# Optimization experiments

Hardware: AMD Instinct MI355X
Metric: run time of the kernel (lower is better)

Reference implementation:

```python
import jax, jax.numpy as jnp
import numpy as np

B, S, D, H, HD, I, L = 1, 2048, 1024, 16, 64, 2816, 2
EPS = 1e-5
ROPE_BASE = 10000.0


def rmsnorm(x, w):
    return x * jax.lax.rsqrt(jnp.mean(x * x, axis=-1, keepdims=True) + EPS) * w


def precompute_freqs_cis():
    # matches precompute_freqs_cis: [S, HD//2, 2] = (cos, sin)
    freqs = 1.0 / (ROPE_BASE ** (jnp.arange(0, HD, 2, dtype=jnp.float32) / HD))
    ang = jnp.outer(jnp.arange(S, dtype=jnp.float32), freqs)
    return jnp.stack([jnp.cos(ang), jnp.sin(ang)], axis=-1)


def apply_rope(x, fc):
    # x: [B,S,H,HD]; fc: [S,HD//2,2] -> interleaved pair rotation
    xs = x.reshape(*x.shape[:-1], HD // 2, 2)
    f = fc[None, :, None]  # [1,S,1,HD//2,2]
    out = jnp.stack([
        xs[..., 0] * f[..., 0] - xs[..., 1] * f[..., 1],
        xs[..., 1] * f[..., 0] + xs[..., 0] * f[..., 1],
    ], axis=-1)
    return out.reshape(x.shape)


def setup_inputs() -> dict:
    key = jax.random.key(0)
    ks = jax.random.split(key, 6)
    p = lambda k, shape: jax.random.normal(k, shape, jnp.float32) * 0.02
    return {
        "x": jax.random.normal(ks[0], (B, S, D), jnp.float32),
        "wqkv": p(ks[1], (L, 3 * H * HD, D)),
        "wo": p(ks[2], (L, D, H * HD)),
        "w1": p(ks[3], (L, I, D)),
        "w2": p(ks[4], (L, D, I)),
        "w3": p(ks[5], (L, I, D)),
        "attn_norm_w": jnp.ones((L, D), jnp.float32),
        "ffn_norm_w": jnp.ones((L, D), jnp.float32),
        "attn_ls": 0.01 * jnp.ones((L, D), jnp.float32),
        "ffn_ls": 0.01 * jnp.ones((L, D), jnp.float32),
        "final_norm_w": jnp.ones((D,), jnp.float32),
    }


def reference(x, wqkv, wo, w1, w2, w3, attn_norm_w, ffn_norm_w, attn_ls, ffn_ls, final_norm_w):
    fc = precompute_freqs_cis()
    causal = jnp.tril(jnp.ones((S, S), dtype=bool))  # [S,S]
    scale = 1.0 / np.sqrt(HD).astype(np.float32)
    h = x
    for l in range(L):
        # --- attention block ---
        xn = rmsnorm(h, attn_norm_w[l])
        qkv = xn @ wqkv[l].T  # [B,S,3*H*HD]
        q, k, v = jnp.split(qkv, 3, axis=-1)
        q = apply_rope(q.reshape(B, S, H, HD), fc)
        k = apply_rope(k.reshape(B, S, H, HD), fc)
        v = v.reshape(B, S, H, HD)
        scores = jnp.einsum('bqhd,bkhd->bhqk', q, k) * scale
        scores = jnp.where(causal, scores, jnp.finfo(scores.dtype).min)
        attn = jax.nn.softmax(scores, axis=-1)
        y = jnp.einsum('bhqk,bkhd->bqhd', attn, v).reshape(B, S, H * HD)
        h = h + (y @ wo[l].T) * attn_ls[l]
        # --- feed-forward block (SwiGLU) ---
        xn = rmsnorm(h, ffn_norm_w[l])
        ff = (jax.nn.silu(xn @ w1[l].T) * (xn @ w3[l].T)) @ w2[l].T
        h = h + ff * ffn_ls[l]
    return rmsnorm(h, final_norm_w)
```

## Files before the change

kernel.cpp:

```cpp
#include <hip/hip_runtime.h>
#include <math.h>

#define SEQ 2048
#define DIM 1024
#define NH 16
#define HDIM 64
#define IDIM 2816
#define NL 2

typedef __attribute__((ext_vector_type(8))) short bf16x8;
typedef __attribute__((ext_vector_type(4))) float f32x4;

__device__ __forceinline__ unsigned short f2bf(float f) {
    unsigned int u = __float_as_uint(f);
    u = (u + 0x7fffu + ((u >> 16) & 1u)) >> 16;
    return (unsigned short)u;
}
__device__ __forceinline__ float bf2f(unsigned short u) {
    return __uint_as_float((unsigned int)u << 16);
}

__device__ __forceinline__ void gl_lds16(const void* g, void* l) {
    __builtin_amdgcn_global_load_lds(
        (const __attribute__((address_space(1))) unsigned int*)g,
        (__attribute__((address_space(3))) unsigned int*)l, 16, 0, 0);
}

#define WAITVM(n) asm volatile("s_waitcnt vmcnt(" #n ")" ::: "memory")
#define BARRIER_PIN()                       \
    do {                                    \
        __builtin_amdgcn_s_barrier();       \
        __builtin_amdgcn_sched_barrier(0);  \
    } while (0)

template <bool BF16OUT>
__global__ __launch_bounds__(256) void rmsnorm_kernel(const float* __restrict__ in,
                                                      const float* __restrict__ w,
                                                      void* __restrict__ out) {
    const int row = blockIdx.x;
    const int t = threadIdx.x;
    const float4 v = ((const float4*)(in + (size_t)row * DIM))[t];
    float ss = v.x * v.x + v.y * v.y + v.z * v.z + v.w * v.w;
#pragma unroll
    for (int m = 1; m < 64; m <<= 1) ss += __shfl_xor(ss, m);
    __shared__ float red[4];
    if ((t & 63) == 0) red[t >> 6] = ss;
    __syncthreads();
    const float tot = red[0] + red[1] + red[2] + red[3];
    const float r = 1.0f / sqrtf(tot * (1.0f / DIM) + 1e-5f);
    const float4 wv = ((const float4*)w)[t];
    float o0 = v.x * r * wv.x, o1 = v.y * r * wv.y;
    float o2 = v.z * r * wv.z, o3 = v.w * r * wv.w;
    if (BF16OUT) {
        ushort4 o = {f2bf(o0), f2bf(o1), f2bf(o2), f2bf(o3)};
        ((ushort4*)((unsigned short*)out + (size_t)row * DIM))[t] = o;
    } else {
        float4 o = {o0, o1, o2, o3};
        ((float4*)((float*)out + (size_t)row * DIM))[t] = o;
    }
}

#define WQKV_OFF 0
#define WO_OFF   3145728
#define W1_OFF   4194304
#define W3_OFF   7077888
#define W2_OFF   9961472
#define WTOT     12845056

__global__ __launch_bounds__(256) void convert_weights_kernel(
    const float* __restrict__ wqkv, const float* __restrict__ wo,
    const float* __restrict__ w1, const float* __restrict__ w3,
    const float* __restrict__ w2, unsigned short* __restrict__ out) {
    const size_t i8 = ((size_t)blockIdx.x * 256 + threadIdx.x) * 8;
    const float* src;
    size_t local;
    if (i8 < WO_OFF)      { src = wqkv; local = i8 - WQKV_OFF; }
    else if (i8 < W1_OFF) { src = wo;   local = i8 - WO_OFF; }
    else if (i8 < W3_OFF) { src = w1;   local = i8 - W1_OFF; }
    else if (i8 < W2_OFF) { src = w3;   local = i8 - W3_OFF; }
    else                  { src = w2;   local = i8 - W2_OFF; }
    const float4 v0 = *(const float4*)(src + local);
    const float4 v1 = *(const float4*)(src + local + 4);
    ushort4 o0 = {f2bf(v0.x), f2bf(v0.y), f2bf(v0.z), f2bf(v0.w)};
    ushort4 o1 = {f2bf(v1.x), f2bf(v1.y), f2bf(v1.z), f2bf(v1.w)};
    *(ushort4*)(out + i8) = o0;
    *(ushort4*)(out + i8 + 4) = o1;
}

template <int EPI, int BM, int BN, int KSPLIT>
__global__ __launch_bounds__(256) void mfma_gemm(
    const unsigned short* __restrict__ A,
    const unsigned short* __restrict__ B,
    const unsigned short* __restrict__ Bhi, int nsplit,
    float* __restrict__ Cf,
    unsigned short* __restrict__ Cb,
    const float* __restrict__ ls,
    int N, int K) {
    constexpr int MI = BM / 32;
    constexpr int NJ = BN / 32;
    constexpr int L = (BM + BN) / 32;
    static_assert(L == 6 || L == 8, "WAITVM literals cover L=6,8");
    __shared__ unsigned short As[2][BM * 64];
    __shared__ unsigned short Bs[2][BN * 64];

    const int tid = threadIdx.x;

    const int nwg = gridDim.x * gridDim.y;
    const int orig = blockIdx.y * gridDim.x + blockIdx.x;
    const int swz = (orig & 7) * (nwg >> 3) + (orig >> 3);
    const int bx = swz / gridDim.y;
    const int by = swz % gridDim.y;
    const int m0 = by * BM;
    const int ncol0 = bx * BN;

    const unsigned short* Bp = B;
    int n0 = ncol0;
    if (n0 >= nsplit) { Bp = Bhi; n0 -= nsplit; }

    const int Koff = (KSPLIT > 1) ? blockIdx.z * (K / KSPLIT) : 0;

    const int r0 = tid >> 3;
    const int cswz = (tid & 7) ^ (r0 & 7);
    const unsigned short* Ag = A + (size_t)(m0 + r0) * K + Koff + cswz * 8;
    const unsigned short* Bg = Bp + (size_t)(n0 + r0) * K + Koff + cswz * 8;

    const int lane = tid & 63;
    const int wid = tid >> 6;
    const int wr = (wid >> 1) * (BM / 2);
    const int wc = (wid & 1) * (BN / 2);
    const int fr = lane & 15;
    const int hi = lane >> 4;

    f32x4 acc[MI][NJ] = {};

    auto stage = [&](int buf, int kk) {
#pragma unroll
        for (int q = 0; q < BM / 32; ++q)
            gl_lds16(Ag + (size_t)(q * 32) * K + kk, &As[buf][q * 2048 + tid * 8]);
#pragma unroll
        for (int q = 0; q < BN / 32; ++q)
            gl_lds16(Bg + (size_t)(q * 32) * K + kk, &Bs[buf][q * 2048 + tid * 8]);
    };

    auto frag = [&](const unsigned short* base, int R, int c) -> bf16x8 {
        return *(const bf16x8*)&base[R * 64 + ((c ^ (R & 7)) << 3)];
    };

    auto compute_tile = [&](int buf) {
        bf16x8 a[MI][2], b[NJ][2];
#pragma unroll
        for (int m = 0; m < MI; ++m)
#pragma unroll
            for (int kw = 0; kw < 2; ++kw)
                a[m][kw] = frag(As[buf], wr + m * 16 + fr, kw * 4 + hi);
#pragma unroll
        for (int n = 0; n < NJ; ++n)
#pragma unroll
            for (int kw = 0; kw < 2; ++kw)
                b[n][kw] = frag(Bs[buf], wc + n * 16 + fr, kw * 4 + hi);
        __builtin_amdgcn_s_setprio(1);
#pragma unroll
        for (int kw = 0; kw < 2; ++kw)
#pragma unroll
            for (int m = 0; m < MI; ++m)
#pragma unroll
                for (int n = 0; n < NJ; ++n)
                    acc[m][n] = __builtin_amdgcn_mfma_f32_16x16x32_bf16(
                        a[m][kw], b[n][kw], acc[m][n], 0, 0, 0);
        __builtin_amdgcn_s_setprio(0);
    };

    const int NT = K / KSPLIT / 64;

    stage(0, 0);
    stage(1, 64);

    int buf = 0;
    for (int t = 0; t < NT - 1; ++t) {
        if constexpr (L == 6) WAITVM(6); else WAITVM(8);
        BARRIER_PIN();
        compute_tile(buf);
        asm volatile("s_waitcnt lgkmcnt(0)" ::: "memory");
        BARRIER_PIN();
        if (t + 2 < NT) stage(buf, (t + 2) * 64);
        buf ^= 1;
    }
    WAITVM(0);
    BARRIER_PIN();
    compute_tile(buf);

    const int erow = m0 + wr + hi * 4;
    const int ecol = ncol0 + wc + fr;
#pragma unroll
    for (int m = 0; m < MI; ++m) {
#pragma unroll
        for (int n = 0; n < NJ; ++n) {
            const f32x4 v = acc[m][n];
            const int row = erow + m * 16;
            const int col = ecol + n * 16;
            if (EPI == 1) {
                const float lv = ls[col];
#pragma unroll
                for (int j = 0; j < 4; ++j) {
                    float* p = Cf + (size_t)(row + j) * N + col;
                    if (KSPLIT > 1) atomicAdd(p, v[j] * lv);
                    else            *p = *p + v[j] * lv;
                }
            } else {
#pragma unroll
                for (int j = 0; j < 4; ++j)
                    Cb[(size_t)(row + j) * N + col] = f2bf(v[j]);
            }
        }
    }
}

__global__ __launch_bounds__(256) void silu_mul_kernel(
    const unsigned short* __restrict__ c13,
    unsigned short* __restrict__ outp) {
    const size_t e8 = ((size_t)blockIdx.x * 256 + threadIdx.x) * 8;
    const int m = (int)(e8 / IDIM);
    const int i = (int)(e8 % IDIM);
    const unsigned short* g = c13 + (size_t)m * (2 * IDIM) + i;
    const bf16x8 gv = *(const bf16x8*)g;
    const bf16x8 uv = *(const bf16x8*)(g + IDIM);
    unsigned short o[8];
#pragma unroll
    for (int j = 0; j < 8; ++j) {
        const float x = bf2f((unsigned short)gv[j]);
        const float u = bf2f((unsigned short)uv[j]);
        o[j] = f2bf(x / (1.0f + __expf(-x)) * u);
    }
    *(bf16x8*)(outp + (size_t)m * IDIM + i) = *(const bf16x8*)o;
}

__global__ __launch_bounds__(256) void rope_split_kernel(
    const unsigned short* __restrict__ qkv,
    unsigned short* __restrict__ Qh,
    unsigned short* __restrict__ Kh,
    unsigned short* __restrict__ Vt) {
    const int st = blockIdx.x;
    const int h = blockIdx.y;
    const int tid = threadIdx.x;
    const int srow = tid >> 2;
    const int scol = (tid & 3) * 16;
    const int s = st * 64 + srow;
    __shared__ unsigned short Vl[64][72];

    const unsigned short* base = qkv + (size_t)s * (3 * DIM) + h * HDIM + scol;

    unsigned short qv[16], kv[16], vv[16];
    *(bf16x8*)&qv[0] = *(const bf16x8*)(base);
    *(bf16x8*)&qv[8] = *(const bf16x8*)(base + 8);
    *(bf16x8*)&kv[0] = *(const bf16x8*)(base + DIM);
    *(bf16x8*)&kv[8] = *(const bf16x8*)(base + DIM + 8);
    *(bf16x8*)&vv[0] = *(const bf16x8*)(base + 2 * DIM);
    *(bf16x8*)&vv[8] = *(const bf16x8*)(base + 2 * DIM + 8);

    const float FC = -0.28782313662425572f;
    unsigned short qo[16], ko[16];
#pragma unroll
    for (int i = 0; i < 8; ++i) {
        const int p = scol / 2 + i;
        const float freq = __expf(FC * (float)p);
        const float ang = (float)s * freq;
        float sn, cs;
        sincosf(ang, &sn, &cs);
        const float q0 = bf2f(qv[2 * i]), q1 = bf2f(qv[2 * i + 1]);
        const float k0 = bf2f(kv[2 * i]), k1 = bf2f(kv[2 * i + 1]);
        qo[2 * i]     = f2bf(q0 * cs - q1 * sn);
        qo[2 * i + 1] = f2bf(q1 * cs + q0 * sn);
        ko[2 * i]     = f2bf(k0 * cs - k1 * sn);
        ko[2 * i + 1] = f2bf(k1 * cs + k0 * sn);
    }
    unsigned short* qdst = Qh + ((size_t)h * SEQ + s) * HDIM + scol;
    unsigned short* kdst = Kh + ((size_t)h * SEQ + s) * HDIM + scol;
    *(bf16x8*)qdst = *(const bf16x8*)&qo[0];
    *(bf16x8*)(qdst + 8) = *(const bf16x8*)&qo[8];
    *(bf16x8*)kdst = *(const bf16x8*)&ko[0];
    *(bf16x8*)(kdst + 8) = *(const bf16x8*)&ko[8];

#pragma unroll
    for (int i = 0; i < 16; ++i) Vl[scol + i][srow] = vv[i];
    __syncthreads();
    const int d = tid >> 2;
    const int c0 = (tid & 3) * 16;
    unsigned short* vdst = Vt + ((size_t)h * HDIM + d) * SEQ + st * 64 + c0;
    *(bf16x8*)vdst = *(const bf16x8*)&Vl[d][c0];
    *(bf16x8*)(vdst + 8) = *(const bf16x8*)&Vl[d][c0 + 8];
}

__global__ __launch_bounds__(256) void attn_mfma_kernel(
    const unsigned short* __restrict__ Qh,
    const unsigned short* __restrict__ Kh,
    const unsigned short* __restrict__ Vt,
    unsigned short* __restrict__ y) {
    const int h = blockIdx.x;
    const int qt = blockIdx.y;
    const int qb = (qt < 16) ? qt : 47 - qt;

    __shared__ unsigned short Kl[2][64][72];
    __shared__ unsigned short Vl[2][64][72];
    __shared__ unsigned short Pl[64][72];

    const int tid = threadIdx.x;
    const int lane = tid & 63;
    const int w = tid >> 6;
    const int fr = lane & 15;
    const int fk = (lane >> 4) * 8;
    const int rg = (lane >> 4) * 4;
    const int srow = tid >> 2;
    const int sc8 = (tid & 3) * 8;

    bf16x8 qa[2];
    {
        const unsigned short* qsrc =
            Qh + ((size_t)h * SEQ + qb * 64 + w * 16 + fr) * HDIM;
        qa[0] = *(const bf16x8*)(qsrc + fk);
        qa[1] = *(const bf16x8*)(qsrc + 32 + fk);
    }

    bf16x8 kr0, kr1, vr0, vr1;
    {
        const unsigned short* ks = Kh + ((size_t)h * SEQ + srow) * HDIM + sc8;
        kr0 = *(const bf16x8*)ks;
        kr1 = *(const bf16x8*)(ks + 32);
        const unsigned short* vs = Vt + ((size_t)h * HDIM + srow) * SEQ + sc8;
        vr0 = *(const bf16x8*)vs;
        vr1 = *(const bf16x8*)(vs + 32);
    }

    float l_[4] = {0.0f, 0.0f, 0.0f, 0.0f};
    f32x4 O[4] = {};

    for (int kb = 0; kb <= qb; ++kb) {
        const int cur = kb & 1;
        if (kb > 0) __syncthreads();
        *(bf16x8*)&Kl[cur][srow][sc8] = kr0;
        *(bf16x8*)&Kl[cur][srow][sc8 + 32] = kr1;
        *(bf16x8*)&Vl[cur][srow][sc8] = vr0;
        *(bf16x8*)&Vl[cur][srow][sc8 + 32] = vr1;
        __syncthreads();

        if (kb < qb) {
            const unsigned short* ks = Kh + ((size_t)h * SEQ + (kb + 1) * 64 + srow) * HDIM + sc8;
            kr0 = *(const bf16x8*)ks;
            kr1 = *(const bf16x8*)(ks + 32);
            const unsigned short* vs = Vt + ((size_t)h * HDIM + srow) * SEQ + (kb + 1) * 64 + sc8;
            vr0 = *(const bf16x8*)vs;
            vr1 = *(const bf16x8*)(vs + 32);
        }

        f32x4 sa[4] = {};
        __builtin_amdgcn_s_setprio(1);
#pragma unroll
        for (int ks2 = 0; ks2 < 2; ++ks2)
#pragma unroll
            for (int n = 0; n < 4; ++n) {
                const bf16x8 kf = *(const bf16x8*)&Kl[cur][n * 16 + fr][ks2 * 32 + fk];
                sa[n] = __builtin_amdgcn_mfma_f32_16x16x32_bf16(qa[ks2], kf, sa[n], 0, 0, 0);
            }
        __builtin_amdgcn_s_setprio(0);

        const bool diag = (kb == qb);
#pragma unroll
        for (int n = 0; n < 4; ++n) {
            const int col = n * 16 + fr;
#pragma unroll
            for (int j = 0; j < 4; ++j) {
                const float sv = sa[n][j] * 0.125f;
                float e = __expf(fminf(sv, 30.0f));
                if (diag && col > rg + j) e = 0.0f;
                l_[j] += e;
                Pl[w * 16 + rg + j][col] = f2bf(e);
            }
        }

        __builtin_amdgcn_s_setprio(1);
#pragma unroll
        for (int ks2 = 0; ks2 < 2; ++ks2) {
            const bf16x8 pa = *(const bf16x8*)&Pl[w * 16 + fr][ks2 * 32 + fk];
#pragma unroll
            for (int nd = 0; nd < 4; ++nd) {
                const bf16x8 vf = *(const bf16x8*)&Vl[cur][nd * 16 + fr][ks2 * 32 + fk];
                O[nd] = __builtin_amdgcn_mfma_f32_16x16x32_bf16(pa, vf, O[nd], 0, 0, 0);
            }
        }
        __builtin_amdgcn_s_setprio(0);
    }

#pragma unroll
    for (int j = 0; j < 4; ++j) {
#pragma unroll
        for (int msk = 1; msk < 16; msk <<= 1) l_[j] += __shfl_xor(l_[j], msk);
    }

#pragma unroll
    for (int j = 0; j < 4; ++j) {
        const float inv = 1.0f / l_[j];
        unsigned short* dst = y + (size_t)(qb * 64 + w * 16 + rg + j) * DIM + h * HDIM + fr;
#pragma unroll
        for (int nd = 0; nd < 4; ++nd)
            dst[nd * 16] = f2bf(O[nd][j] * inv);
    }
}

extern "C" void kernel_launch(void* const* d_in, const int* in_sizes, int n_in,
                              void* d_out, int out_size, void* d_ws, size_t ws_size,
                              hipStream_t stream) {
    const float* x            = (const float*)d_in[0];
    const float* wqkv         = (const float*)d_in[1];
    const float* wo           = (const float*)d_in[2];
    const float* w1           = (const float*)d_in[3];
    const float* w2           = (const float*)d_in[4];
    const float* w3           = (const float*)d_in[5];
    const float* attn_norm_w  = (const float*)d_in[6];
    const float* ffn_norm_w   = (const float*)d_in[7];
    const float* attn_ls      = (const float*)d_in[8];
    const float* ffn_ls       = (const float*)d_in[9];
    const float* final_norm_w = (const float*)d_in[10];
    float* out = (float*)d_out;

    char* ws = (char*)d_ws;
    float*          h     = (float*)ws;
    unsigned short* xnb   = (unsigned short*)(ws + 8388608);
    unsigned short* yb    = (unsigned short*)(ws + 12582912);
    unsigned short* qkvb  = (unsigned short*)(ws + 16777216);
    unsigned short* Qhb   = (unsigned short*)(ws + 29360128);
    unsigned short* Khb   = (unsigned short*)(ws + 33554432);
    unsigned short* Vtb   = (unsigned short*)(ws + 37748736);
    unsigned short* c13   = (unsigned short*)(ws + 16777216);
    unsigned short* ffb   = (unsigned short*)(ws + 41943040);
    unsigned short* wbuf  = (unsigned short*)(ws + 46137344);

    unsigned short* wqkv_b = wbuf + WQKV_OFF;
    unsigned short* wo_b   = wbuf + WO_OFF;
    unsigned short* w1_b   = wbuf + W1_OFF;
    unsigned short* w3_b   = wbuf + W3_OFF;
    unsigned short* w2_b   = wbuf + W2_OFF;

    const int BIG = 1 << 30;

    hipMemcpyAsync(h, x, (size_t)SEQ * DIM * sizeof(float),
                   hipMemcpyDeviceToDevice, stream);

    for (int l = 0; l < NL; ++l) {
        convert_weights_kernel<<<WTOT / 2048, 256, 0, stream>>>(
            wqkv + (size_t)l * 3 * DIM * DIM, wo + (size_t)l * DIM * DIM,
            w1 + (size_t)l * IDIM * DIM, w3 + (size_t)l * IDIM * DIM,
            w2 + (size_t)l * DIM * IDIM, wbuf);

        rmsnorm_kernel<true><<<SEQ, 256, 0, stream>>>(h, attn_norm_w + l * DIM, xnb);
        mfma_gemm<3, 128, 128, 1><<<dim3(3 * DIM / 128, SEQ / 128), 256, 0, stream>>>(
            xnb, wqkv_b, nullptr, BIG, nullptr, qkvb, nullptr, 3 * DIM, DIM);
        rope_split_kernel<<<dim3(SEQ / 64, NH), 256, 0, stream>>>(qkvb, Qhb, Khb, Vtb);
        attn_mfma_kernel<<<dim3(NH, SEQ / 64), 256, 0, stream>>>(Qhb, Khb, Vtb, yb);
        mfma_gemm<1, 64, 128, 2><<<dim3(DIM / 128, SEQ / 64, 2), 256, 0, stream>>>(
            yb, wo_b, nullptr, BIG, h, nullptr, attn_ls + l * DIM, DIM, DIM);

        rmsnorm_kernel<true><<<SEQ, 256, 0, stream>>>(h, ffn_norm_w + l * DIM, xnb);
        mfma_gemm<3, 128, 128, 1><<<dim3(2 * IDIM / 128, SEQ / 128), 256, 0, stream>>>(
            xnb, w1_b, w3_b, IDIM, nullptr, c13, nullptr, 2 * IDIM, DIM);
        silu_mul_kernel<<<SEQ * IDIM / 2048, 256, 0, stream>>>(c13, ffb);
        mfma_gemm<1, 64, 128, 2><<<dim3(DIM / 128, SEQ / 64, 2), 256, 0, stream>>>(
            ffb, w2_b, nullptr, BIG, h, nullptr, ffn_ls + l * DIM, DIM, IDIM);
    }

    rmsnorm_kernel<false><<<SEQ, 256, 0, stream>>>(h, final_norm_w, out);
}
```

Baseline: 359.6 us.

## Fuse w1/w3 GEMM with SiLU-multiply epilogue into one dual-accumulator kernel

Replaces the concatenated w1|w3 GEMM and the separate silu_mul kernel with one kernel. It stages A, B1 and B3 tiles in LDS and keeps two accumulator sets per wave, then applies silu(g)*u in the epilogue and writes bf16 directly to the FFN input buffer. This removes the round trip of the intermediate c13 tensor through global memory and one kernel launch per layer. In exchange it doubles accumulator registers, which may lower occupancy, and it launches half as many workgroups, which can worsen tail balance across CUs.

```diff
diff --git a/kernel.cpp b/kernel.cpp
--- a/kernel.cpp
+++ b/kernel.cpp
@@ -215,23 +215,125 @@
     }
 }
 
-__global__ __launch_bounds__(256) void silu_mul_kernel(
-    const unsigned short* __restrict__ c13,
-    unsigned short* __restrict__ outp) {
-    const size_t e8 = ((size_t)blockIdx.x * 256 + threadIdx.x) * 8;
-    const int m = (int)(e8 / IDIM);
-    const int i = (int)(e8 % IDIM);
-    const unsigned short* g = c13 + (size_t)m * (2 * IDIM) + i;
-    const bf16x8 gv = *(const bf16x8*)g;
-    const bf16x8 uv = *(const bf16x8*)(g + IDIM);
-    unsigned short o[8];
-#pragma unroll
-    for (int j = 0; j < 8; ++j) {
-        const float x = bf2f((unsigned short)gv[j]);
-        const float u = bf2f((unsigned short)uv[j]);
-        o[j] = f2bf(x / (1.0f + __expf(-x)) * u);
-    }
-    *(bf16x8*)(outp + (size_t)m * IDIM + i) = *(const bf16x8*)o;
+__global__ __launch_bounds__(256) void mfma_gemm_fused13(
+    const unsigned short* __restrict__ A,
+    const unsigned short* __restrict__ B1,
+    const unsigned short* __restrict__ B3,
+    unsigned short* __restrict__ Out,
+    int N, int K) {
+    __shared__ unsigned short As[2][128 * 32];
+    __shared__ unsigned short Bs[2][128 * 32];
+    __shared__ unsigned short B2s[2][128 * 32];
+
+    const int tid = threadIdx.x;
+
+    const int nwg = gridDim.x * gridDim.y;
+    const int orig = blockIdx.y * gridDim.x + blockIdx.x;
+    const int swz = (orig & 7) * (nwg >> 3) + (orig >> 3);
+    const int bx = swz / gridDim.y;
+    const int by = swz % gridDim.y;
+    const int m0 = by * 128;
+    const int n0 = bx * 128;
+
+    const int uc = (tid & 7) ^ ((tid >> 3) & 7);
+    const int srow = 2 * (tid >> 3) + (uc >> 2);
+    const int skof = (uc & 3) * 8;
+    const unsigned short* Ag = A + (size_t)(m0 + srow) * K + skof;
+    const unsigned short* B1g = B1 + (size_t)(n0 + srow) * K + skof;
+    const unsigned short* B3g = B3 + (size_t)(n0 + srow) * K + skof;
+
+    const int lane = tid & 63;
+    const int wid = tid >> 6;
+    const int wr = (wid >> 1) * 64;
+    const int wc = (wid & 1) * 64;
+    const int fr = lane & 15;
+    const int hi = lane >> 4;
+
+    f32x4 acc[4][4] = {};
+    f32x4 acc2[4][4] = {};
+
+    auto stage = [&](int buf, int kk) {
+#pragma unroll
+        for (int q = 0; q < 2; ++q)
+            gl_lds16(Ag + (size_t)(q * 64) * K + kk, &As[buf][q * 2048 + tid * 8]);
+#pragma unroll
+        for (int q = 0; q < 2; ++q)
+            gl_lds16(B1g + (size_t)(q * 64) * K + kk, &Bs[buf][q * 2048 + tid * 8]);
+#pragma unroll
+        for (int q = 0; q < 2; ++q)
+            gl_lds16(B3g + (size_t)(q * 64) * K + kk, &B2s[buf][q * 2048 + tid * 8]);
+    };
+
+    auto frag = [&](const unsigned short* base, int R, int c) -> bf16x8 {
+        const int vr = R >> 1;
+        const int slot = (((R & 1) * 4 + c) ^ (vr & 7));
+        return *(const bf16x8*)&base[vr * 64 + slot * 8];
+    };
+
+    auto compute_tile = [&](int buf) {
+        bf16x8 a[4], b[4], b2[4];
+#pragma unroll
+        for (int m = 0; m < 4; ++m)
+            a[m] = frag(As[buf], wr + m * 16 + fr, hi);
+#pragma unroll
+        for (int n = 0; n < 4; ++n)
+            b[n] = frag(Bs[buf], wc + n * 16 + fr, hi);
+#pragma unroll
+        for (int n = 0; n < 4; ++n)
+            b2[n] = frag(B2s[buf], wc + n * 16 + fr, hi);
+        __builtin_amdgcn_s_setprio(1);
+#pragma unroll
+        for (int m = 0; m < 4; ++m)
+#pragma unroll
+            for (int n = 0; n < 4; ++n)
+                acc[m][n] = __builtin_amdgcn_mfma_f32_16x16x32_bf16(
+                    a[m], b[n], acc[m][n], 0, 0, 0);
+#pragma unroll
+        for (int m = 0; m < 4; ++m)
+#pragma unroll
+            for (int n = 0; n < 4; ++n)
+                acc2[m][n] = __builtin_amdgcn_mfma_f32_16x16x32_bf16(
+                    a[m], b2[n], acc2[m][n], 0, 0, 0);
+        __builtin_amdgcn_s_setprio(0);
+    };
+
+    const int NT = K / 32;
+
+    stage(0, 0);
+    stage(1, 32);
+
+    int buf = 0;
+    for (int t = 0; t < NT - 1; ++t) {
+        WAITVM(6);
+        BARRIER_PIN();
+        compute_tile(buf);
+        asm volatile("s_waitcnt lgkmcnt(0)" ::: "memory");
+        BARRIER_PIN();
+        if (t + 2 < NT) stage(buf, (t + 2) * 32);
+        buf ^= 1;
+    }
+    WAITVM(0);
+    BARRIER_PIN();
+    compute_tile(buf);
+
+    const int erow = m0 + wr + hi * 4;
+    const int ecol = n0 + wc + fr;
+#pragma unroll
+    for (int m = 0; m < 4; ++m) {
+#pragma unroll
+        for (int n = 0; n < 4; ++n) {
+            const f32x4 g = acc[m][n];
+            const f32x4 u = acc2[m][n];
+            const int row = erow + m * 16;
+            const int col = ecol + n * 16;
+#pragma unroll
+            for (int j = 0; j < 4; ++j) {
+                const float x = g[j];
+                Out[(size_t)(row + j) * N + col] =
+                    f2bf(x / (1.0f + __expf(-x)) * u[j]);
+            }
+        }
+    }
 }
 
 __global__ __launch_bounds__(256) void rope_split_kernel(
@@ -429,7 +531,6 @@
     unsigned short* Qhb   = (unsigned short*)(ws + 29360128);
     unsigned short* Khb   = (unsigned short*)(ws + 33554432);
     unsigned short* Vtb   = (unsigned short*)(ws + 37748736);
-    unsigned short* c13   = (unsigned short*)(ws + 16777216);
     unsigned short* ffb   = (unsigned short*)(ws + 41943040);
     unsigned short* wbuf  = (unsigned short*)(ws + 46137344);
 
@@ -459,9 +560,8 @@
             yb, wo_b, nullptr, BIG, h, nullptr, attn_ls + l * DIM, DIM, DIM);
 
         rmsnorm_kernel<true><<<SEQ, 256, 0, stream>>>(h, ffn_norm_w + l * DIM, xnb);
-        mfma_gemm<3, 128, 128, 1><<<dim3(2 * IDIM / 128, SEQ / 128), 256, 0, stream>>>(
-            xnb, w1_b, w3_b, IDIM, nullptr, c13, nullptr, 2 * IDIM, DIM);
-        silu_mul_kernel<<<SEQ * IDIM / 2048, 256, 0, stream>>>(c13, ffb);
+        mfma_gemm_fused13<<<dim3(IDIM / 128, SEQ / 128), 256, 0, stream>>>(
+            xnb, w1_b, w3_b, ffb, IDIM, DIM);
         mfma_gemm<1, 64, 128, 2><<<dim3(DIM / 128, SEQ / 64, 2), 256, 0, stream>>>(
             ffb, w2_b, nullptr, BIG, h, nullptr, ffn_ls + l * DIM, DIM, IDIM);
     }
```

Result: faster. 350.9 us (-2.4%).
